# Kernel optimization log

Measured on AMD Instinct MI355X. Metric: run time of the kernel, lower is better.

The kernel has to match this reference:

```python
import jax, jax.numpy as jnp
import numpy as np

N, S, B, C = 512, 28, 3, 80
D = B * 5 + C
LAMBDA_COORD, LAMBDA_NOOBJ = 5.0, 0.5
BATCH_SIZE = float(N)


def setup_inputs() -> dict:
    key = jax.random.key(0)
    k1, k2, k3, k4, k5 = jax.random.split(key, 5)
    # predictions: positive so sqrt(w), sqrt(h) is defined (as the torch code assumes)
    pred = jax.random.uniform(k1, (N, S, S, D), dtype=jnp.float32, minval=0.05, maxval=1.0)
    # YOLOv1-style target: objectness in first B channels, gt box repeated B times, then C classes
    obj = (jax.random.uniform(k2, (N, S, S)) > 0.7).astype(jnp.float32)
    xy = jax.random.uniform(k3, (N, S, S, 2), minval=0.1, maxval=0.9)
    wh = jax.random.uniform(k4, (N, S, S, 2), minval=0.05, maxval=0.8)
    box = jnp.concatenate([xy, wh], axis=-1)                      # [N,S,S,4]
    boxes = jnp.tile(box, (1, 1, 1, B))                           # [N,S,S,B*4] (x,y,w,h repeated)
    conf = jnp.broadcast_to(obj[..., None], (N, S, S, B))         # [N,S,S,B]
    cls = jax.random.uniform(k5, (N, S, S, C)) * obj[..., None]
    target = jnp.concatenate([conf, boxes, cls], axis=-1)         # [N,S,S,D]
    return {"pred_tensor": pred, "target_tensor": target}


def _corners(b):
    # convert_CxCyWH_to_X1Y1X2Y2: center divided by S, +/- half extent
    xy = b[..., :2] / S
    half = b[..., 2:] * 0.5
    return xy - half, xy + half


def reference(pred_tensor, target_tensor):
    dt = pred_tensor.dtype
    tconf0 = target_tensor[..., 0]
    obj = (tconf0 > 0).astype(dt)       # [N,S,S]
    noobj = (tconf0 == 0).astype(dt)

    conf_p = pred_tensor[..., :B]                                   # [N,S,S,B]
    box_p = pred_tensor[..., B:5 * B].reshape(N, S, S, B, 4)        # [N,S,S,B,4]
    cls_p = pred_tensor[..., 5 * B:]                                # [N,S,S,C]
    conf_t = target_tensor[..., :B]
    box_t = target_tensor[..., B:5 * B].reshape(N, S, S, B, 4)
    cls_t = target_tensor[..., 5 * B:]
    gt_box = box_t[..., 0, :]                                       # cell gt box [N,S,S,4]

    # no-obj confidence loss (sum over all no-object cells, all B confidences)
    no_obj_loss = jnp.sum(noobj[..., None] * (conf_p - conf_t) ** 2)

    # IoU of each of the B predicted boxes vs the gt box, per cell
    p1, p2 = _corners(box_p)                                        # [N,S,S,B,2]
    t1, t2 = _corners(gt_box)                                       # [N,S,S,2]
    lt = jnp.maximum(p1, t1[..., None, :])
    rb = jnp.minimum(p2, t2[..., None, :])
    wh = jnp.maximum(rb - lt, 0.0)
    inter = wh[..., 0] * wh[..., 1]                                 # [N,S,S,B]
    area_p = (p2 - p1)[..., 0] * (p2 - p1)[..., 1]
    area_t = ((t2 - t1)[..., 0] * (t2 - t1)[..., 1])[..., None]
    iou = inter / (area_p + area_t - inter)                         # [N,S,S,B]

    # responsible box per object cell (argmax ties -> first index, same as torch .max)
    best = jnp.argmax(iou, axis=-1)
    onehot = jax.nn.one_hot(best, B, dtype=dt)                      # [N,S,S,B]
    active = onehot * obj[..., None]
    not_active = (1.0 - onehot) * obj[..., None]

    contain_loss = jnp.sum(active * (conf_p - iou) ** 2)
    not_contain_loss = jnp.sum(not_active * conf_p ** 2)

    # localization: xy MSE + sqrt(wh) MSE on responsible boxes
    d_xy = box_p[..., :2] - box_t[..., :2]
    d_wh = jnp.sqrt(box_p[..., 2:]) - jnp.sqrt(box_t[..., 2:])
    location_loss = jnp.sum(active[..., None] * d_xy ** 2) + jnp.sum(active[..., None] * d_wh ** 2)

    # class loss over object cells
    cls_loss = jnp.sum(obj[..., None] * (cls_p - cls_t) ** 2)

    total = (LAMBDA_COORD * location_loss + contain_loss + not_contain_loss
             + LAMBDA_NOOBJ * no_obj_loss + cls_loss) / BATCH_SIZE
    return total
```

## Files before the change

kernel.cpp:

```cpp
#include <hip/hip_runtime.h>

namespace {
constexpr int   kD      = 95;
constexpr int   kCPB    = 64;
constexpr int   kBlocks = 401408 / kCPB;
constexpr int   kF4PB   = kCPB * kD / 4;
constexpr float kS      = 28.0f;
}

typedef float vf4 __attribute__((ext_vector_type(4)));

__device__ __forceinline__ void stage(const vf4 p, const vf4 t, const int i,
                                      vf4* __restrict__ s_d4,
                                      float* __restrict__ s_t)
{
    s_d4[i] = p - t;
    const int v   = i * 4;
    const int cl0 = v / kD;
    const int j0  = v - cl0 * kD;
    if (j0 < 7 || j0 >= kD - 3) {
        #pragma unroll
        for (int c = 0; c < 4; ++c) {
            const int  jj   = j0 + c;
            const bool wrap = (jj >= kD);
            const int  j    = wrap ? jj - kD : jj;
            const int  cl   = cl0 + (wrap ? 1 : 0);
            if (j < 7) s_t[cl * 7 + j] = t[c];
        }
    }
}

__device__ __forceinline__ float compute_iou(
    float bx, float by, float bw, float bh,
    float t1x, float t1y, float t2x, float t2y, float area_t)
{
    const float p1x = bx * (1.0f / kS) - bw * 0.5f;
    const float p1y = by * (1.0f / kS) - bh * 0.5f;
    const float p2x = bx * (1.0f / kS) + bw * 0.5f;
    const float p2y = by * (1.0f / kS) + bh * 0.5f;
    const float ltx = fmaxf(p1x, t1x);
    const float lty = fmaxf(p1y, t1y);
    const float rbx = fminf(p2x, t2x);
    const float rby = fminf(p2y, t2y);
    const float wx  = fmaxf(rbx - ltx, 0.0f);
    const float wy  = fmaxf(rby - lty, 0.0f);
    const float inter  = wx * wy;
    const float area_p = (p2x - p1x) * (p2y - p1y);
    return inter / (area_p + area_t - inter);
}

__global__ __launch_bounds__(256)
void yolo_loss_kernel(const float* __restrict__ pred,
                      const float* __restrict__ targ,
                      float* __restrict__ partials)
{
    __shared__ vf4   s_d4[kF4PB];
    __shared__ float s_t[kCPB * 7];
    __shared__ float s_red[4];
    float* s_d = reinterpret_cast<float*>(s_d4);

    const int tid = threadIdx.x;
    const size_t base4 = (size_t)blockIdx.x * kF4PB;
    const vf4* p4 = reinterpret_cast<const vf4*>(pred) + base4;
    const vf4* t4 = reinterpret_cast<const vf4*>(targ) + base4;

    const int i0 = tid,        i1 = tid + 256;
    const int i2 = tid + 512,  i3 = tid + 768;
    const int i4 = tid + 1024, i5 = tid + 1280;
    const bool tail = (tid < 240);

    const vf4 P0 = __builtin_nontemporal_load(&p4[i0]);  const vf4 T0 = t4[i0];
    const vf4 P1 = __builtin_nontemporal_load(&p4[i1]);  const vf4 T1 = t4[i1];
    const vf4 P2 = __builtin_nontemporal_load(&p4[i2]);  const vf4 T2 = t4[i2];
    const vf4 P3 = __builtin_nontemporal_load(&p4[i3]);  const vf4 T3 = t4[i3];
    const vf4 P4 = __builtin_nontemporal_load(&p4[i4]);  const vf4 T4 = t4[i4];
    vf4 P5, T5;
    if (tail) {
        P5 = __builtin_nontemporal_load(&p4[i5]);
        T5 = t4[i5];
    }

    stage(P0, T0, i0, s_d4, s_t);
    stage(P1, T1, i1, s_d4, s_t);
    stage(P2, T2, i2, s_d4, s_t);
    stage(P3, T3, i3, s_d4, s_t);
    stage(P4, T4, i4, s_d4, s_t);
    if (tail) stage(P5, T5, i5, s_d4, s_t);

    __syncthreads();

    const int lane = tid & 63;
    const int wv   = tid >> 6;
    float acc = 0.0f;
    {
        const int  base = lane * kD;
        const bool obj  = (s_t[lane * 7 + 0] > 0.0f);
        float s2a = 0.0f, s2b = 0.0f;
        const int jb = 15 + 20 * wv;
        #pragma unroll
        for (int j = 0; j < 20; j += 2) {
            const float a = s_d[base + jb + j];
            const float b = s_d[base + jb + j + 1];
            s2a = fmaf(a, a, s2a);
            s2b = fmaf(b, b, s2b);
        }
        acc = obj ? (s2a + s2b) : 0.0f;
    }

    if (wv == 0) {
        const int base = lane * kD;
        const float tc0 = s_t[lane * 7 + 0];
        const bool  obj = (tc0 > 0.0f);

        const float d0 = s_d[base + 0];
        const float d1 = s_d[base + 1];
        const float d2 = s_d[base + 2];

        if (!obj) {
            acc += 0.5f * (d0 * d0 + d1 * d1 + d2 * d2);
        } else {
            const float gx = s_t[lane * 7 + 3], gy = s_t[lane * 7 + 4];
            const float gw = s_t[lane * 7 + 5], gh = s_t[lane * 7 + 6];

            const float cp0 = d0 + 1.0f, cp1 = d1 + 1.0f, cp2 = d2 + 1.0f;
            const float bx0 = s_d[base + 3]  + gx, by0 = s_d[base + 4]  + gy;
            const float bw0 = s_d[base + 5]  + gw, bh0 = s_d[base + 6]  + gh;
            const float bx1 = s_d[base + 7]  + gx, by1 = s_d[base + 8]  + gy;
            const float bw1 = s_d[base + 9]  + gw, bh1 = s_d[base + 10] + gh;
            const float bx2 = s_d[base + 11] + gx, by2 = s_d[base + 12] + gy;
            const float bw2 = s_d[base + 13] + gw, bh2 = s_d[base + 14] + gh;

            const float t1x = gx * (1.0f / kS) - gw * 0.5f;
            const float t1y = gy * (1.0f / kS) - gh * 0.5f;
            const float t2x = gx * (1.0f / kS) + gw * 0.5f;
            const float t2y = gy * (1.0f / kS) + gh * 0.5f;
            const float area_t = (t2x - t1x) * (t2y - t1y);

            const float iou0 = compute_iou(bx0, by0, bw0, bh0, t1x, t1y, t2x, t2y, area_t);
            const float iou1 = compute_iou(bx1, by1, bw1, bh1, t1x, t1y, t2x, t2y, area_t);
            const float iou2 = compute_iou(bx2, by2, bw2, bh2, t1x, t1y, t2x, t2y, area_t);

            int   best = 0;
            float biou = iou0;
            if (iou1 > biou) { best = 1; biou = iou1; }
            if (iou2 > biou) { best = 2; biou = iou2; }

            const float cb  = (best == 0) ? cp0 : ((best == 1) ? cp1 : cp2);
            const float sbx = (best == 0) ? bx0 : ((best == 1) ? bx1 : bx2);
            const float sby = (best == 0) ? by0 : ((best == 1) ? by1 : by2);
            const float sbw = (best == 0) ? bw0 : ((best == 1) ? bw1 : bw2);
            const float sbh = (best == 0) ? bh0 : ((best == 1) ? bh1 : bh2);

            const float dc = cb - biou;
            acc += dc * dc;

            acc += ((best == 0) ? 0.0f : cp0 * cp0)
                 + ((best == 1) ? 0.0f : cp1 * cp1)
                 + ((best == 2) ? 0.0f : cp2 * cp2);

            const float dx = sbx - gx;
            const float dy = sby - gy;
            const float dw = sqrtf(sbw) - sqrtf(gw);
            const float dh = sqrtf(sbh) - sqrtf(gh);
            acc += 5.0f * (dx * dx + dy * dy + dw * dw + dh * dh);
        }
    }

    #pragma unroll
    for (int off = 32; off > 0; off >>= 1)
        acc += __shfl_down(acc, off, 64);

    if (lane == 0) s_red[wv] = acc;
    __syncthreads();
    if (tid == 0)
        partials[blockIdx.x] = s_red[0] + s_red[1] + s_red[2] + s_red[3];
}

__global__ __launch_bounds__(1024)
void reduce_kernel(const float* __restrict__ partials, float* __restrict__ out)
{
    __shared__ float s_red[16];
    float a = 0.0f;
    for (int i = threadIdx.x; i < kBlocks; i += 1024) a += partials[i];
    #pragma unroll
    for (int off = 32; off > 0; off >>= 1)
        a += __shfl_down(a, off, 64);
    const int wave = threadIdx.x >> 6;
    const int lane = threadIdx.x & 63;
    if (lane == 0) s_red[wave] = a;
    __syncthreads();
    if (threadIdx.x == 0) {
        float s = 0.0f;
        #pragma unroll
        for (int w = 0; w < 16; ++w) s += s_red[w];
        out[0] = s * (1.0f / 512.0f);
    }
}

extern "C" void kernel_launch(void* const* d_in, const int* in_sizes, int n_in,
                              void* d_out, int out_size, void* d_ws, size_t ws_size,
                              hipStream_t stream) {
    const float* pred = (const float*)d_in[0];
    const float* targ = (const float*)d_in[1];
    float* out = (float*)d_out;
    float* ws  = (float*)d_ws;

    yolo_loss_kernel<<<kBlocks, 256, 0, stream>>>(pred, targ, ws);
    reduce_kernel<<<1, 1024, 0, stream>>>(ws, out);
}
```

Baseline: 52.34 us.

## Process four tiles per block with double-buffered LDS and load-compute overlap

Each block now handles four 64-cell tiles instead of one and cuts the grid by four. Shared memory is double-buffered so the global loads for the next tile are issued before the compute on the previously staged tile, overlapping memory latency with arithmetic. The per-tile reduction is also amortized across more work. In exchange, each block uses twice the LDS and more registers, which lowers occupancy, and the grid has fewer blocks to spread across CUs.

```diff
diff --git a/kernel.cpp b/kernel.cpp
--- a/kernel.cpp
+++ b/kernel.cpp
@@ -3,16 +3,37 @@
 namespace {
 constexpr int   kD      = 95;
 constexpr int   kCPB    = 64;
-constexpr int   kBlocks = 401408 / kCPB;
-constexpr int   kF4PB   = kCPB * kD / 4;
+constexpr int   kTPB    = 4;
+constexpr int   kTiles  = 401408 / kCPB;
+constexpr int   kGrid   = kTiles / kTPB;
+constexpr int   kF4PT   = kCPB * kD / 4;
 constexpr float kS      = 28.0f;
 }
 
 typedef float vf4 __attribute__((ext_vector_type(4)));
 
-__device__ __forceinline__ void stage(const vf4 p, const vf4 t, const int i,
-                                      vf4* __restrict__ s_d4,
-                                      float* __restrict__ s_t)
+struct TileRegs { vf4 P0,P1,P2,P3,P4,P5, T0,T1,T2,T3,T4,T5; };
+
+__device__ __forceinline__ void load_tile(const float* __restrict__ pred,
+                                          const float* __restrict__ targ,
+                                          int tile, int tid, TileRegs& R)
+{
+    const vf4* p4 = reinterpret_cast<const vf4*>(pred) + (size_t)tile * kF4PT;
+    const vf4* t4 = reinterpret_cast<const vf4*>(targ) + (size_t)tile * kF4PT;
+    R.P0 = __builtin_nontemporal_load(&p4[tid]);         R.T0 = t4[tid];
+    R.P1 = __builtin_nontemporal_load(&p4[tid +  256]);  R.T1 = t4[tid +  256];
+    R.P2 = __builtin_nontemporal_load(&p4[tid +  512]);  R.T2 = t4[tid +  512];
+    R.P3 = __builtin_nontemporal_load(&p4[tid +  768]);  R.T3 = t4[tid +  768];
+    R.P4 = __builtin_nontemporal_load(&p4[tid + 1024]);  R.T4 = t4[tid + 1024];
+    if (tid < 240) {
+        R.P5 = __builtin_nontemporal_load(&p4[tid + 1280]);
+        R.T5 = t4[tid + 1280];
+    }
+}
+
+__device__ __forceinline__ void stage1(const vf4 p, const vf4 t, const int i,
+                                       vf4* __restrict__ s_d4,
+                                       float* __restrict__ s_t)
 {
     s_d4[i] = p - t;
     const int v   = i * 4;
@@ -30,6 +51,18 @@
     }
 }
 
+__device__ __forceinline__ void stage_tile(const TileRegs& R, int tid,
+                                           vf4* __restrict__ s_d4,
+                                           float* __restrict__ s_t)
+{
+    stage1(R.P0, R.T0, tid,        s_d4, s_t);
+    stage1(R.P1, R.T1, tid +  256, s_d4, s_t);
+    stage1(R.P2, R.T2, tid +  512, s_d4, s_t);
+    stage1(R.P3, R.T3, tid +  768, s_d4, s_t);
+    stage1(R.P4, R.T4, tid + 1024, s_d4, s_t);
+    if (tid < 240) stage1(R.P5, R.T5, tid + 1280, s_d4, s_t);
+}
+
 __device__ __forceinline__ float compute_iou(
     float bx, float by, float bw, float bh,
     float t1x, float t1y, float t2x, float t2y, float area_t)
@@ -49,52 +82,14 @@
     return inter / (area_p + area_t - inter);
 }
 
-__global__ __launch_bounds__(256)
-void yolo_loss_kernel(const float* __restrict__ pred,
-                      const float* __restrict__ targ,
-                      float* __restrict__ partials)
-{
-    __shared__ vf4   s_d4[kF4PB];
-    __shared__ float s_t[kCPB * 7];
-    __shared__ float s_red[4];
-    float* s_d = reinterpret_cast<float*>(s_d4);
-
-    const int tid = threadIdx.x;
-    const size_t base4 = (size_t)blockIdx.x * kF4PB;
-    const vf4* p4 = reinterpret_cast<const vf4*>(pred) + base4;
-    const vf4* t4 = reinterpret_cast<const vf4*>(targ) + base4;
-
-    const int i0 = tid,        i1 = tid + 256;
-    const int i2 = tid + 512,  i3 = tid + 768;
-    const int i4 = tid + 1024, i5 = tid + 1280;
-    const bool tail = (tid < 240);
-
-    const vf4 P0 = __builtin_nontemporal_load(&p4[i0]);  const vf4 T0 = t4[i0];
-    const vf4 P1 = __builtin_nontemporal_load(&p4[i1]);  const vf4 T1 = t4[i1];
-    const vf4 P2 = __builtin_nontemporal_load(&p4[i2]);  const vf4 T2 = t4[i2];
-    const vf4 P3 = __builtin_nontemporal_load(&p4[i3]);  const vf4 T3 = t4[i3];
-    const vf4 P4 = __builtin_nontemporal_load(&p4[i4]);  const vf4 T4 = t4[i4];
-    vf4 P5, T5;
-    if (tail) {
-        P5 = __builtin_nontemporal_load(&p4[i5]);
-        T5 = t4[i5];
-    }
-
-    stage(P0, T0, i0, s_d4, s_t);
-    stage(P1, T1, i1, s_d4, s_t);
-    stage(P2, T2, i2, s_d4, s_t);
-    stage(P3, T3, i3, s_d4, s_t);
-    stage(P4, T4, i4, s_d4, s_t);
-    if (tail) stage(P5, T5, i5, s_d4, s_t);
-
-    __syncthreads();
-
-    const int lane = tid & 63;
-    const int wv   = tid >> 6;
-    float acc = 0.0f;
+__device__ __forceinline__ float phaseB(const float* __restrict__ s_d,
+                                        const float* __restrict__ s_t,
+                                        int lane, int wv)
+{
+    float acc;
+    const int  base = lane * kD;
+    const bool obj  = (s_t[lane * 7 + 0] > 0.0f);
     {
-        const int  base = lane * kD;
-        const bool obj  = (s_t[lane * 7 + 0] > 0.0f);
         float s2a = 0.0f, s2b = 0.0f;
         const int jb = 15 + 20 * wv;
         #pragma unroll
@@ -108,10 +103,6 @@
     }
 
     if (wv == 0) {
-        const int base = lane * kD;
-        const float tc0 = s_t[lane * 7 + 0];
-        const bool  obj = (tc0 > 0.0f);
-
         const float d0 = s_d[base + 0];
         const float d1 = s_d[base + 1];
         const float d2 = s_d[base + 2];
@@ -165,6 +156,46 @@
             acc += 5.0f * (dx * dx + dy * dy + dw * dw + dh * dh);
         }
     }
+    return acc;
+}
+
+__global__ __launch_bounds__(256)
+void yolo_loss_kernel(const float* __restrict__ pred,
+                      const float* __restrict__ targ,
+                      float* __restrict__ partials)
+{
+    __shared__ vf4   s_d4A[kF4PT], s_d4B[kF4PT];
+    __shared__ float s_tA[kCPB * 7], s_tB[kCPB * 7];
+    __shared__ float s_red[4];
+
+    const int tid  = threadIdx.x;
+    const int lane = tid & 63;
+    const int wv   = tid >> 6;
+    const int t0   = blockIdx.x * kTPB;
+
+    float acc = 0.0f;
+    TileRegs R;
+
+    load_tile(pred, targ, t0, tid, R);
+    stage_tile(R, tid, s_d4A, s_tA);
+    __syncthreads();
+
+    #pragma unroll
+    for (int k = 1; k < kTPB; ++k) {
+        load_tile(pred, targ, t0 + k, tid, R);
+        const bool prevA = ((k - 1) & 1) == 0;
+        acc += phaseB(prevA ? (const float*)s_d4A : (const float*)s_d4B,
+                      prevA ? s_tA : s_tB, lane, wv);
+        if (k & 1) stage_tile(R, tid, s_d4B, s_tB);
+        else       stage_tile(R, tid, s_d4A, s_tA);
+        __syncthreads();
+    }
+
+    {
+        const bool lastA = ((kTPB - 1) & 1) == 0;
+        acc += phaseB(lastA ? (const float*)s_d4A : (const float*)s_d4B,
+                      lastA ? s_tA : s_tB, lane, wv);
+    }
 
     #pragma unroll
     for (int off = 32; off > 0; off >>= 1)
@@ -181,7 +212,7 @@
 {
     __shared__ float s_red[16];
     float a = 0.0f;
-    for (int i = threadIdx.x; i < kBlocks; i += 1024) a += partials[i];
+    for (int i = threadIdx.x; i < kGrid; i += 1024) a += partials[i];
     #pragma unroll
     for (int off = 32; off > 0; off >>= 1)
         a += __shfl_down(a, off, 64);
@@ -205,6 +236,6 @@
     float* out = (float*)d_out;
     float* ws  = (float*)d_ws;
 
-    yolo_loss_kernel<<<kBlocks, 256, 0, stream>>>(pred, targ, ws);
+    yolo_loss_kernel<<<kGrid, 256, 0, stream>>>(pred, targ, ws);
     reduce_kernel<<<1, 1024, 0, stream>>>(ws, out);
 }
```

After: 55.22 us. 5.5% more time.
